# Performance work log

Hardware: AMD Instinct MI355X
Metric: run time of the kernel (lower is better)

Reference implementation:

```python
import jax, jax.numpy as jnp
import numpy as np

N, E = 50000, 1600000
C_IN, C_H, C_OUT = 36, 64, 64
EPS = 1e-16  # PyG softmax denominator epsilon


def setup_inputs() -> dict:
    key = jax.random.key(0)
    ks = jax.random.split(key, 48)
    inp = {}
    inp["features"] = jax.random.normal(ks[0], (N, C_IN), dtype=jnp.float32)
    inp["edge_attr"] = jax.random.uniform(ks[1], (E, 1), dtype=jnp.float32)
    inp["edge_index"] = jax.random.randint(ks[2], (2, E), 0, N, dtype=jnp.int32)
    dims = [(C_IN, C_H), (C_H, C_H), (C_H, C_H), (C_H, C_OUT)]
    i = 3
    for l, (din, dout) in enumerate(dims, 1):
        s = 1.0 / np.sqrt(din)
        inp[f"Wl{l}"] = jax.random.normal(ks[i], (din, dout), jnp.float32) * s; i += 1
        inp[f"bl{l}"] = jax.random.normal(ks[i], (dout,), jnp.float32) * 0.02; i += 1
        inp[f"Wr{l}"] = jax.random.normal(ks[i], (din, dout), jnp.float32) * s; i += 1
        inp[f"br{l}"] = jax.random.normal(ks[i], (dout,), jnp.float32) * 0.02; i += 1
        inp[f"We{l}"] = jax.random.normal(ks[i], (1, dout), jnp.float32); i += 1
        inp[f"att{l}"] = jax.random.normal(ks[i], (dout,), jnp.float32) * s; i += 1
        inp[f"bo{l}"] = jax.random.normal(ks[i], (dout,), jnp.float32) * 0.02; i += 1
    mlp = [(C_OUT, C_OUT // 2, "m1"), (C_OUT // 2, C_OUT // 4, "m2"), (C_OUT // 4, 1, "m3")]
    for din, dout, tag in mlp:
        s = 1.0 / np.sqrt(din)
        inp[f"W{tag}"] = jax.random.normal(ks[i], (din, dout), jnp.float32) * s; i += 1
        inp[f"b{tag}"] = jax.random.normal(ks[i], (dout,), jnp.float32) * 0.02; i += 1
    return inp


def gatv2_conv(x, src, dst, edge_attr, Wl, bl, Wr, br, We, att, bo):
    """Single-head GATv2Conv with edge features (PyG semantics)."""
    xl = x @ Wl + bl                      # [N, dout] source transform
    xr = x @ Wr + br                      # [N, dout] target transform
    ea = edge_attr @ We                   # [E, dout]
    e = jax.nn.leaky_relu(xl[src] + xr[dst] + ea, 0.2)  # [E, dout]
    score = e @ att                       # [E]
    # segment softmax over edges sharing a destination node
    m = jax.ops.segment_max(score, dst, num_segments=N)
    a = jnp.exp(score - m[dst])
    denom = jax.ops.segment_sum(a, dst, num_segments=N)
    alpha = a / (denom[dst] + EPS)
    out = jax.ops.segment_sum(xl[src] * alpha[:, None], dst, num_segments=N)
    return out + bo


def reference(features, edge_attr, edge_index,
              Wl1, bl1, Wr1, br1, We1, att1, bo1,
              Wl2, bl2, Wr2, br2, We2, att2, bo2,
              Wl3, bl3, Wr3, br3, We3, att3, bo3,
              Wl4, bl4, Wr4, br4, We4, att4, bo4,
              Wm1, bm1, Wm2, bm2, Wm3, bm3):
    src, dst = edge_index[0], edge_index[1]
    x = jax.nn.relu(gatv2_conv(features, src, dst, edge_attr, Wl1, bl1, Wr1, br1, We1, att1, bo1))
    x = jax.nn.relu(gatv2_conv(x, src, dst, edge_attr, Wl2, bl2, Wr2, br2, We2, att2, bo2))
    x = jax.nn.relu(gatv2_conv(x, src, dst, edge_attr, Wl3, bl3, Wr3, br3, We3, att3, bo3))
    x = jax.nn.relu(gatv2_conv(x, src, dst, edge_attr, Wl4, bl4, Wr4, br4, We4, att4, bo4))
    x = jnp.mean(x, axis=-2)              # graph readout -> [C_OUT]
    x = jax.nn.relu(x @ Wm1 + bm1)
    x = jax.nn.relu(x @ Wm2 + bm2)
    return x @ Wm3 + bm3                  # [1]
```

## Files before the change

### kernel.cpp

```cpp
#include <hip/hip_runtime.h>


__device__ __forceinline__ float readlane_f(float v, int l) {
  return __int_as_float(__builtin_amdgcn_readlane(__float_as_int(v), l));
}
__device__ __forceinline__ int rfl(int v) { return __builtin_amdgcn_readfirstlane(v); }

__device__ __forceinline__ void row_to_lds(const float* g, float* l) {
  __builtin_amdgcn_global_load_lds((const __attribute__((address_space(1))) void*)g,
                                   (__attribute__((address_space(3))) void*)l,
                                   4, 0, 0);
}

__global__ void k_hist(const int* __restrict__ dst, int* __restrict__ deg, int E) {
  int e = blockIdx.x * blockDim.x + threadIdx.x;
  if (e < E) atomicAdd(&deg[dst[e]], 1);
}

__global__ void __launch_bounds__(256) k_scanA(const int* __restrict__ deg,
                                               int* __restrict__ bsum, int n) {
  __shared__ int ws[4];
  int tid = threadIdx.x, lane = tid & 63, wv = tid >> 6;
  int base = blockIdx.x * 1024 + tid;
  int s = 0;
  #pragma unroll
  for (int k = 0; k < 4; k++) {
    int i = base + k * 256;
    if (i < n) s += deg[i];
  }
  #pragma unroll
  for (int o = 32; o > 0; o >>= 1) s += __shfl_xor(s, o, 64);
  if (lane == 0) ws[wv] = s;
  __syncthreads();
  if (tid == 0) bsum[blockIdx.x] = ws[0] + ws[1] + ws[2] + ws[3];
}

__global__ void k_scanB(const int* __restrict__ bsum, int* __restrict__ boffs,
                        int* __restrict__ rowptr, int nb, int n) {
  int lane = threadIdx.x;
  int v = (lane < nb) ? bsum[lane] : 0;
  int x = v;
  #pragma unroll
  for (int o = 1; o < 64; o <<= 1) {
    int t = __shfl_up(x, o, 64);
    if (lane >= o) x += t;
  }
  if (lane < nb) boffs[lane] = x - v;
  if (lane == 63) rowptr[n] = x;
}

__global__ void __launch_bounds__(256) k_scanC(const int* __restrict__ deg,
                                               const int* __restrict__ boffs,
                                               int* __restrict__ rowptr, int n) {
  __shared__ int wtot[4];
  int tid = threadIdx.x, lane = tid & 63, wv = tid >> 6;
  int i0 = blockIdx.x * 1024 + tid * 4;
  int4 v = make_int4(0, 0, 0, 0);
  if (i0 + 3 < n) v = *(const int4*)(deg + i0);
  else {
    if (i0 + 0 < n) v.x = deg[i0 + 0];
    if (i0 + 1 < n) v.y = deg[i0 + 1];
    if (i0 + 2 < n) v.z = deg[i0 + 2];
  }
  int s = v.x + v.y + v.z + v.w;
  int x = s;
  #pragma unroll
  for (int o = 1; o < 64; o <<= 1) {
    int t = __shfl_up(x, o, 64);
    if (lane >= o) x += t;
  }
  if (lane == 63) wtot[wv] = x;
  __syncthreads();
  int wexcl = 0;
  for (int k = 0; k < 4; k++) if (k < wv) wexcl += wtot[k];
  int excl = boffs[blockIdx.x] + wexcl + (x - s);
  int4 o4;
  o4.x = excl; o4.y = o4.x + v.x; o4.z = o4.y + v.y; o4.w = o4.z + v.z;
  if (i0 + 3 < n) *(int4*)(rowptr + i0) = o4;
  else {
    if (i0 + 0 < n) rowptr[i0 + 0] = o4.x;
    if (i0 + 1 < n) rowptr[i0 + 1] = o4.y;
    if (i0 + 2 < n) rowptr[i0 + 2] = o4.z;
  }
}

#define NBK_MAX 256
__global__ void __launch_bounds__(256) k_scatter(
    const int* __restrict__ src, const int* __restrict__ dst,
    const float* __restrict__ ea_in, const int* __restrict__ rowptr,
    int* __restrict__ bcur, uint2* __restrict__ tmp, int E, int nbk) {
  __shared__ int cnt[NBK_MAX];
  __shared__ int cur[NBK_MAX];
  __shared__ int gbase[NBK_MAX];
  __shared__ int sbase[NBK_MAX];
  int tid = threadIdx.x;
  if (tid < nbk) {
    cnt[tid] = 0;
    cur[tid] = 0;
    sbase[tid] = rowptr[tid << 8];
  }
  __syncthreads();
  int base = blockIdx.x * 4096 + tid;
  uint2 rec[16];
  #pragma unroll
  for (int k = 0; k < 16; k++) {
    int e = base + k * 256;
    if (e < E) {
      unsigned d = (unsigned)dst[e];
      rec[k] = make_uint2((d << 16) | (unsigned)src[e],
                          (unsigned)__float_as_int(ea_in[e]));
      atomicAdd(&cnt[d >> 8], 1);
    } else {
      rec[k] = make_uint2(0u, 0u);
    }
  }
  __syncthreads();
  if (tid < nbk) {
    int c = cnt[tid];
    gbase[tid] = (c > 0) ? atomicAdd(&bcur[tid * 16], c) : 0;
  }
  __syncthreads();
  #pragma unroll
  for (int k = 0; k < 16; k++) {
    int e = base + k * 256;
    if (e < E) {
      int b = (int)(rec[k].x >> 24);
      int slot = atomicAdd(&cur[b], 1);
      tmp[sbase[b] + gbase[b] + slot] = rec[k];
    }
  }
}

__global__ void __launch_bounds__(256) k_csr(const int* __restrict__ rowptr,
                                             const uint2* __restrict__ tmp,
                                             int2* __restrict__ pairs, int N) {
  __shared__ int sRP[257];
  __shared__ int cur[256];
  int b = blockIdx.x;
  int n0 = b << 8;
  int tid = threadIdx.x;
  sRP[tid] = rowptr[min(n0 + tid, N)];
  if (tid == 0) sRP[256] = rowptr[min(n0 + 256, N)];
  cur[tid] = 0;
  __syncthreads();
  int lo = sRP[0], hi = sRP[256];
  for (int k = lo + tid; k < hi; k += 256) {
    uint2 rec = tmp[k];
    int local = (int)(rec.x >> 16) - n0;
    int pos = sRP[local] + atomicAdd(&cur[local], 1);
    pairs[pos] = make_int2((int)(rec.x & 0xffffu), (int)rec.y);
  }
}

template <int DIN, int TILES>
__global__ void __launch_bounds__(256) k_transform(
    const float* __restrict__ x, const float* __restrict__ Wl, const float* __restrict__ bl,
    const float* __restrict__ Wr, const float* __restrict__ br,
    float* __restrict__ xl, float* __restrict__ xr, int nNodes) {
  __shared__ __align__(16) float sWl[DIN * 64];
  __shared__ __align__(16) float sWr[DIN * 64];
  __shared__ float sx[16][DIN + 1];
  int tid = threadIdx.x;
  for (int i = tid; i < DIN * 64; i += 256) { sWl[i] = Wl[i]; sWr[i] = Wr[i]; }
  int node = tid >> 4;
  int t4 = (tid & 15) * 4;
  float4 bl4 = *(const float4*)(bl + t4);
  float4 br4 = *(const float4*)(br + t4);
  for (int t = 0; t < TILES; t++) {
    int nb = (blockIdx.x * TILES + t) * 16;
    if (nb >= nNodes) break;
    __syncthreads();
    for (int i = tid; i < 16 * DIN; i += 256) {
      int ln = i / DIN, c = i % DIN;
      int g = nb + ln;
      sx[ln][c] = (g < nNodes) ? x[(size_t)g * DIN + c] : 0.f;
    }
    __syncthreads();
    float4 accl = bl4;
    float4 accr = br4;
    const float* xrow = sx[node];
    #pragma unroll 4
    for (int k = 0; k < DIN; k++) {
      float xv = xrow[k];
      float4 wl = *(const float4*)(sWl + k * 64 + t4);
      float4 wr = *(const float4*)(sWr + k * 64 + t4);
      accl.x = fmaf(xv, wl.x, accl.x); accl.y = fmaf(xv, wl.y, accl.y);
      accl.z = fmaf(xv, wl.z, accl.z); accl.w = fmaf(xv, wl.w, accl.w);
      accr.x = fmaf(xv, wr.x, accr.x); accr.y = fmaf(xv, wr.y, accr.y);
      accr.z = fmaf(xv, wr.z, accr.z); accr.w = fmaf(xv, wr.w, accr.w);
    }
    int g = nb + node;
    if (g < nNodes) {
      *(float4*)(xl + (size_t)g * 64 + t4) = accl;
      *(float4*)(xr + (size_t)g * 64 + t4) = accr;
    }
  }
}

#define SC1(T, EA, OUT) { float u, acc; \
  u = T.x + fmaf(EA, We4.x, xr4.x); u = fmaxf(u, 0.2f * u); acc = at4.x * u; \
  u = T.y + fmaf(EA, We4.y, xr4.y); u = fmaxf(u, 0.2f * u); acc = fmaf(at4.y, u, acc); \
  u = T.z + fmaf(EA, We4.z, xr4.z); u = fmaxf(u, 0.2f * u); acc = fmaf(at4.z, u, acc); \
  u = T.w + fmaf(EA, We4.w, xr4.w); u = fmaxf(u, 0.2f * u); acc = fmaf(at4.w, u, acc); \
  OUT = acc; }

__global__ void __launch_bounds__(256, 5) k_edge(
    const float* __restrict__ xl, const float* __restrict__ xr,
    const int* __restrict__ rowptr, const int2* __restrict__ pairs,
    const float* __restrict__ We, const float* __restrict__ att,
    const float* __restrict__ bo, float* __restrict__ xout, int nNodes) {
  int lane = threadIdx.x & 63;
  int wv = rfl((int)(threadIdx.x >> 6));
  int n = rfl(blockIdx.x * 4 + wv);
  if (n >= nNodes) return;
  int c4 = lane & 15;
  int r  = lane >> 4;
  int cb = c4 * 4;

  float4 We4 = *(const float4*)(We + cb);
  float4 at4 = *(const float4*)(att + cb);
  float4 xr4 = *(const float4*)(xr + (size_t)n * 64 + cb);
  int s0 = rfl(rowptr[n]);
  int s1 = rfl(rowptr[n + 1]);
  int last = s1 - 1;

  float m = -3.0e38f, d = 0.f;
  float4 A = {0.f, 0.f, 0.f, 0.f};

  for (int kb = s0; kb < s1; kb += 16) {
    int cnt = rfl(min(16, s1 - kb));
    int2 p0 = pairs[min(kb + r,      last)];
    int2 p1 = pairs[min(kb + 4 + r,  last)];
    int2 p2 = pairs[min(kb + 8 + r,  last)];
    int2 p3 = pairs[min(kb + 12 + r, last)];
    float ea0 = __int_as_float(p0.y);
    float ea1 = __int_as_float(p1.y);
    float ea2 = __int_as_float(p2.y);
    float ea3 = __int_as_float(p3.y);

    float4 t0 = *(const float4*)(xl + (size_t)(unsigned)p0.x * 64 + cb);
    float4 t1 = *(const float4*)(xl + (size_t)(unsigned)p1.x * 64 + cb);
    float4 t2 = *(const float4*)(xl + (size_t)(unsigned)p2.x * 64 + cb);
    float4 t3 = *(const float4*)(xl + (size_t)(unsigned)p3.x * 64 + cb);

    float sc0, sc1, sc2, sc3;
    SC1(t0, ea0, sc0)
    SC1(t1, ea1, sc1)
    SC1(t2, ea2, sc2)
    SC1(t3, ea3, sc3)

    #pragma unroll
    for (int o = 1; o <= 8; o <<= 1) {
      sc0 += __shfl_xor(sc0, o, 64);
      sc1 += __shfl_xor(sc1, o, 64);
      sc2 += __shfl_xor(sc2, o, 64);
      sc3 += __shfl_xor(sc3, o, 64);
    }
    sc0 = (r < cnt)      ? sc0 : -3.0e38f;
    sc1 = (4 + r < cnt)  ? sc1 : -3.0e38f;
    sc2 = (8 + r < cnt)  ? sc2 : -3.0e38f;
    sc3 = (12 + r < cnt) ? sc3 : -3.0e38f;

    float mc = fmaxf(fmaxf(sc0, sc1), fmaxf(sc2, sc3));
    mc = fmaxf(mc, __shfl_xor(mc, 16, 64));
    mc = fmaxf(mc, __shfl_xor(mc, 32, 64));
    float newm = fmaxf(m, mc);
    float rf = __expf(m - newm);
    float a0 = __expf(sc0 - newm);
    float a1 = __expf(sc1 - newm);
    float a2 = __expf(sc2 - newm);
    float a3 = __expf(sc3 - newm);
    float ds = (a0 + a1) + (a2 + a3);
    ds += __shfl_xor(ds, 16, 64);
    ds += __shfl_xor(ds, 32, 64);
    d = d * rf + ds;
    m = newm;

    A.x = fmaf(a0, t0.x, A.x * rf); A.y = fmaf(a0, t0.y, A.y * rf);
    A.z = fmaf(a0, t0.z, A.z * rf); A.w = fmaf(a0, t0.w, A.w * rf);
    A.x = fmaf(a1, t1.x, A.x); A.y = fmaf(a1, t1.y, A.y);
    A.z = fmaf(a1, t1.z, A.z); A.w = fmaf(a1, t1.w, A.w);
    A.x = fmaf(a2, t2.x, A.x); A.y = fmaf(a2, t2.y, A.y);
    A.z = fmaf(a2, t2.z, A.z); A.w = fmaf(a2, t2.w, A.w);
    A.x = fmaf(a3, t3.x, A.x); A.y = fmaf(a3, t3.y, A.y);
    A.z = fmaf(a3, t3.z, A.z); A.w = fmaf(a3, t3.w, A.w);
  }

  A.x += __shfl_xor(A.x, 16, 64); A.y += __shfl_xor(A.y, 16, 64);
  A.z += __shfl_xor(A.z, 16, 64); A.w += __shfl_xor(A.w, 16, 64);
  A.x += __shfl_xor(A.x, 32, 64); A.y += __shfl_xor(A.y, 32, 64);
  A.z += __shfl_xor(A.z, 32, 64); A.w += __shfl_xor(A.w, 32, 64);

  float inv = 1.f / (d + 1e-16f);
  if (r == 0) {
    float4 bo4 = *(const float4*)(bo + cb);
    float4 o4;
    o4.x = fmaxf(fmaf(A.x, inv, bo4.x), 0.f);
    o4.y = fmaxf(fmaf(A.y, inv, bo4.y), 0.f);
    o4.z = fmaxf(fmaf(A.z, inv, bo4.z), 0.f);
    o4.w = fmaxf(fmaf(A.w, inv, bo4.w), 0.f);
    *(float4*)(xout + (size_t)n * 64 + cb) = o4;
  }
}

__global__ void k_mean(const float* __restrict__ x, double* __restrict__ meanbuf, int nNodes) {
  __shared__ float sacc[256];
  int lane = threadIdx.x & 63;
  int wv = threadIdx.x >> 6;
  int gw = blockIdx.x * 4 + wv;
  int stride = gridDim.x * 4;
  float acc = 0.f;
  for (int n = gw; n < nNodes; n += stride) acc += x[(size_t)n * 64 + lane];
  sacc[threadIdx.x] = acc;
  __syncthreads();
  if (threadIdx.x < 64) {
    float a = sacc[threadIdx.x] + sacc[threadIdx.x + 64] + sacc[threadIdx.x + 128] + sacc[threadIdx.x + 192];
    atomicAdd(&meanbuf[lane], (double)a);
  }
}

__global__ void k_mlp(const double* __restrict__ meanbuf,
                      const float* __restrict__ Wm1, const float* __restrict__ bm1,
                      const float* __restrict__ Wm2, const float* __restrict__ bm2,
                      const float* __restrict__ Wm3, const float* __restrict__ bm3,
                      float* __restrict__ out, double invN) {
  __shared__ float xm[64];
  __shared__ float h1[32];
  __shared__ float h2[16];
  int t = threadIdx.x;
  xm[t] = (float)(meanbuf[t] * invN);
  __syncthreads();
  if (t < 32) {
    float a = bm1[t];
    for (int c = 0; c < 64; c++) a = fmaf(xm[c], Wm1[c * 32 + t], a);
    h1[t] = fmaxf(a, 0.f);
  }
  __syncthreads();
  if (t < 16) {
    float a = bm2[t];
    for (int c = 0; c < 32; c++) a = fmaf(h1[c], Wm2[c * 16 + t], a);
    h2[t] = fmaxf(a, 0.f);
  }
  __syncthreads();
  if (t == 0) {
    float a = bm3[0];
    for (int c = 0; c < 16; c++) a = fmaf(h2[c], Wm3[c], a);
    out[0] = a;
  }
}

extern "C" void kernel_launch(void* const* d_in, const int* in_sizes, int n_in,
                              void* d_out, int out_size, void* d_ws, size_t ws_size,
                              hipStream_t stream) {
  (void)n_in; (void)out_size; (void)ws_size;
  const int N = in_sizes[0] / 36;
  const int E = in_sizes[1];

  const float* feat = (const float*)d_in[0];
  const float* eat  = (const float*)d_in[1];
  const int*   eidx = (const int*)d_in[2];
  const int* src = eidx;
  const int* dst = eidx + E;

  const float* L[4][7];
  for (int l = 0; l < 4; l++)
    for (int j = 0; j < 7; j++) L[l][j] = (const float*)d_in[3 + l * 7 + j];
  const float* Wm1 = (const float*)d_in[31];
  const float* bm1 = (const float*)d_in[32];
  const float* Wm2 = (const float*)d_in[33];
  const float* bm2 = (const float*)d_in[34];
  const float* Wm3 = (const float*)d_in[35];
  const float* bm3 = (const float*)d_in[36];

  const int NBK = (N + 255) >> 8;

  char* ws = (char*)d_ws;
  size_t off = 0;
  auto alloc = [&](size_t bytes) {
    off = (off + 511) & ~(size_t)511;
    void* p = ws + off;
    off += bytes;
    return p;
  };
  int*    deg     = (int*)alloc((size_t)N * 4);
  int*    bcur    = (int*)alloc((size_t)NBK * 16 * 4);
  double* meanbuf = (double*)alloc(64 * 8);
  size_t zero_bytes = off;
  int*    rowptr  = (int*)alloc((size_t)(N + 1) * 4);
  int*    bsum    = (int*)alloc(64 * 4);
  int*    boffs   = (int*)alloc(64 * 4);
  int2*   pairs   = (int2*)alloc((size_t)E * 8);
  float*  xA      = (float*)alloc((size_t)N * 64 * 4);
  float*  xB      = (float*)alloc((size_t)N * 64 * 4);
  float*  xC      = (float*)alloc((size_t)N * 64 * 4);
  uint2*  tmp     = (uint2*)xC;

  hipMemsetAsync(d_ws, 0, zero_bytes, stream);

  const int TILES = 4;
  int egrid = (E + 255) / 256;
  int sgrid = (E + 4095) / 4096;
  int tgrid = (N + 16 * TILES - 1) / (16 * TILES);
  int ngrid = (N + 3) / 4;
  int nb = (N + 1023) / 1024;

  k_hist<<<egrid, 256, 0, stream>>>(dst, deg, E);
  k_scanA<<<nb, 256, 0, stream>>>(deg, bsum, N);
  k_scanB<<<1, 64, 0, stream>>>(bsum, boffs, rowptr, nb, N);
  k_scanC<<<nb, 256, 0, stream>>>(deg, boffs, rowptr, N);
  k_scatter<<<sgrid, 256, 0, stream>>>(src, dst, eat, rowptr, bcur, tmp, E, NBK);
  k_csr<<<NBK, 256, 0, stream>>>(rowptr, tmp, pairs, N);

  for (int l = 0; l < 4; l++) {
    if (l == 0)
      k_transform<36, TILES><<<tgrid, 256, 0, stream>>>(feat, L[0][0], L[0][1], L[0][2], L[0][3], xA, xB, N);
    else
      k_transform<64, TILES><<<tgrid, 256, 0, stream>>>(xC, L[l][0], L[l][1], L[l][2], L[l][3], xA, xB, N);
    k_edge<<<ngrid, 256, 0, stream>>>(xA, xB, rowptr, pairs,
                                      L[l][4], L[l][5], L[l][6], xC, N);
  }

  k_mean<<<256, 256, 0, stream>>>(xC, meanbuf, N);
  k_mlp<<<1, 64, 0, stream>>>(meanbuf, Wm1, bm1, Wm2, bm2, Wm3, bm3, (float*)d_out, 1.0 / (double)N);
}
```

Baseline: 577.8 us.

## Replace per-node degree histogram and scan with bucket counts plus per-block local scan

Removes the global per-node atomic histogram and three-kernel scan used to build CSR row pointers. Instead, each block counts edges per 256-node bucket in LDS and a single-block scan produces bucket offsets. The CSR kernel then counts and scans per-node degrees locally in LDS and writes rowptr itself. This cuts global atomic traffic and two kernel launches, at the cost of an extra pass over each bucket's records in k_csr.

```diff
diff --git a/kernel.cpp b/kernel.cpp
--- a/kernel.cpp
+++ b/kernel.cpp
@@ -1,93 +1,51 @@
 #include <hip/hip_runtime.h>
 
 
-__device__ __forceinline__ float readlane_f(float v, int l) {
-  return __int_as_float(__builtin_amdgcn_readlane(__float_as_int(v), l));
-}
 __device__ __forceinline__ int rfl(int v) { return __builtin_amdgcn_readfirstlane(v); }
 
-__device__ __forceinline__ void row_to_lds(const float* g, float* l) {
-  __builtin_amdgcn_global_load_lds((const __attribute__((address_space(1))) void*)g,
-                                   (__attribute__((address_space(3))) void*)l,
-                                   4, 0, 0);
-}
-
-__global__ void k_hist(const int* __restrict__ dst, int* __restrict__ deg, int E) {
-  int e = blockIdx.x * blockDim.x + threadIdx.x;
-  if (e < E) atomicAdd(&deg[dst[e]], 1);
-}
-
-__global__ void __launch_bounds__(256) k_scanA(const int* __restrict__ deg,
-                                               int* __restrict__ bsum, int n) {
-  __shared__ int ws[4];
+#define NBK_MAX 256
+
+__global__ void __launch_bounds__(256) k_bcount(const int* __restrict__ dst,
+                                                int* __restrict__ bkcnt, int E, int nbk) {
+  __shared__ int cnt[NBK_MAX];
+  int tid = threadIdx.x;
+  if (tid < nbk) cnt[tid] = 0;
+  __syncthreads();
+  int base = blockIdx.x * 4096 + tid;
+  #pragma unroll
+  for (int k = 0; k < 16; k++) {
+    int e = base + k * 256;
+    if (e < E) atomicAdd(&cnt[((unsigned)dst[e]) >> 8], 1);
+  }
+  __syncthreads();
+  if (tid < nbk) {
+    int c = cnt[tid];
+    if (c > 0) atomicAdd(&bkcnt[tid * 16], c);
+  }
+}
+
+__global__ void k_bscan(const int* __restrict__ bkcnt, int* __restrict__ boffs,
+                        int nbk, int E) {
+  __shared__ int wsum[4];
   int tid = threadIdx.x, lane = tid & 63, wv = tid >> 6;
-  int base = blockIdx.x * 1024 + tid;
-  int s = 0;
-  #pragma unroll
-  for (int k = 0; k < 4; k++) {
-    int i = base + k * 256;
-    if (i < n) s += deg[i];
-  }
-  #pragma unroll
-  for (int o = 32; o > 0; o >>= 1) s += __shfl_xor(s, o, 64);
-  if (lane == 0) ws[wv] = s;
-  __syncthreads();
-  if (tid == 0) bsum[blockIdx.x] = ws[0] + ws[1] + ws[2] + ws[3];
-}
-
-__global__ void k_scanB(const int* __restrict__ bsum, int* __restrict__ boffs,
-                        int* __restrict__ rowptr, int nb, int n) {
-  int lane = threadIdx.x;
-  int v = (lane < nb) ? bsum[lane] : 0;
+  int v = (tid < nbk) ? bkcnt[tid * 16] : 0;
   int x = v;
   #pragma unroll
   for (int o = 1; o < 64; o <<= 1) {
     int t = __shfl_up(x, o, 64);
     if (lane >= o) x += t;
   }
-  if (lane < nb) boffs[lane] = x - v;
-  if (lane == 63) rowptr[n] = x;
-}
-
-__global__ void __launch_bounds__(256) k_scanC(const int* __restrict__ deg,
-                                               const int* __restrict__ boffs,
-                                               int* __restrict__ rowptr, int n) {
-  __shared__ int wtot[4];
-  int tid = threadIdx.x, lane = tid & 63, wv = tid >> 6;
-  int i0 = blockIdx.x * 1024 + tid * 4;
-  int4 v = make_int4(0, 0, 0, 0);
-  if (i0 + 3 < n) v = *(const int4*)(deg + i0);
-  else {
-    if (i0 + 0 < n) v.x = deg[i0 + 0];
-    if (i0 + 1 < n) v.y = deg[i0 + 1];
-    if (i0 + 2 < n) v.z = deg[i0 + 2];
-  }
-  int s = v.x + v.y + v.z + v.w;
-  int x = s;
-  #pragma unroll
-  for (int o = 1; o < 64; o <<= 1) {
-    int t = __shfl_up(x, o, 64);
-    if (lane >= o) x += t;
-  }
-  if (lane == 63) wtot[wv] = x;
-  __syncthreads();
-  int wexcl = 0;
-  for (int k = 0; k < 4; k++) if (k < wv) wexcl += wtot[k];
-  int excl = boffs[blockIdx.x] + wexcl + (x - s);
-  int4 o4;
-  o4.x = excl; o4.y = o4.x + v.x; o4.z = o4.y + v.y; o4.w = o4.z + v.z;
-  if (i0 + 3 < n) *(int4*)(rowptr + i0) = o4;
-  else {
-    if (i0 + 0 < n) rowptr[i0 + 0] = o4.x;
-    if (i0 + 1 < n) rowptr[i0 + 1] = o4.y;
-    if (i0 + 2 < n) rowptr[i0 + 2] = o4.z;
-  }
-}
-
-#define NBK_MAX 256
+  if (lane == 63) wsum[wv] = x;
+  __syncthreads();
+  int wo = 0;
+  for (int k = 0; k < 4; k++) if (k < wv) wo += wsum[k];
+  if (tid < nbk) boffs[tid] = wo + (x - v);
+  if (tid == 0) boffs[nbk] = E;
+}
+
 __global__ void __launch_bounds__(256) k_scatter(
     const int* __restrict__ src, const int* __restrict__ dst,
-    const float* __restrict__ ea_in, const int* __restrict__ rowptr,
+    const float* __restrict__ ea_in, const int* __restrict__ boffs,
     int* __restrict__ bcur, uint2* __restrict__ tmp, int E, int nbk) {
   __shared__ int cnt[NBK_MAX];
   __shared__ int cur[NBK_MAX];
@@ -97,7 +55,7 @@
   if (tid < nbk) {
     cnt[tid] = 0;
     cur[tid] = 0;
-    sbase[tid] = rowptr[tid << 8];
+    sbase[tid] = boffs[tid];
   }
   __syncthreads();
   int base = blockIdx.x * 4096 + tid;
@@ -131,23 +89,44 @@
   }
 }
 
-__global__ void __launch_bounds__(256) k_csr(const int* __restrict__ rowptr,
+__global__ void __launch_bounds__(256) k_csr(const int* __restrict__ boffs,
                                              const uint2* __restrict__ tmp,
-                                             int2* __restrict__ pairs, int N) {
-  __shared__ int sRP[257];
+                                             int2* __restrict__ pairs,
+                                             int* __restrict__ rowptr, int N) {
+  __shared__ int cnt[256];
+  __shared__ int pref[256];
   __shared__ int cur[256];
+  __shared__ int wsum[4];
   int b = blockIdx.x;
   int n0 = b << 8;
-  int tid = threadIdx.x;
-  sRP[tid] = rowptr[min(n0 + tid, N)];
-  if (tid == 0) sRP[256] = rowptr[min(n0 + 256, N)];
+  int tid = threadIdx.x, lane = tid & 63, wv = tid >> 6;
+  cnt[tid] = 0;
   cur[tid] = 0;
   __syncthreads();
-  int lo = sRP[0], hi = sRP[256];
+  int lo = boffs[b], hi = boffs[b + 1];
+  for (int k = lo + tid; k < hi; k += 256)
+    atomicAdd(&cnt[(int)(tmp[k].x >> 16) - n0], 1);
+  __syncthreads();
+  int v = cnt[tid];
+  int x = v;
+  #pragma unroll
+  for (int o = 1; o < 64; o <<= 1) {
+    int t = __shfl_up(x, o, 64);
+    if (lane >= o) x += t;
+  }
+  if (lane == 63) wsum[wv] = x;
+  __syncthreads();
+  int wo = 0;
+  for (int k = 0; k < 4; k++) if (k < wv) wo += wsum[k];
+  int start = lo + wo + (x - v);
+  pref[tid] = start;
+  int nn = n0 + tid;
+  if (nn <= N) rowptr[nn] = start;
+  __syncthreads();
   for (int k = lo + tid; k < hi; k += 256) {
     uint2 rec = tmp[k];
     int local = (int)(rec.x >> 16) - n0;
-    int pos = sRP[local] + atomicAdd(&cur[local], 1);
+    int pos = pref[local] + atomicAdd(&cur[local], 1);
     pairs[pos] = make_int2((int)(rec.x & 0xffffu), (int)rec.y);
   }
 }
@@ -382,13 +361,12 @@
     off += bytes;
     return p;
   };
-  int*    deg     = (int*)alloc((size_t)N * 4);
+  int*    bkcnt   = (int*)alloc((size_t)NBK * 16 * 4);
   int*    bcur    = (int*)alloc((size_t)NBK * 16 * 4);
   double* meanbuf = (double*)alloc(64 * 8);
   size_t zero_bytes = off;
+  int*    boffs   = (int*)alloc((size_t)(NBK + 1) * 4);
   int*    rowptr  = (int*)alloc((size_t)(N + 1) * 4);
-  int*    bsum    = (int*)alloc(64 * 4);
-  int*    boffs   = (int*)alloc(64 * 4);
   int2*   pairs   = (int2*)alloc((size_t)E * 8);
   float*  xA      = (float*)alloc((size_t)N * 64 * 4);
   float*  xB      = (float*)alloc((size_t)N * 64 * 4);
@@ -398,18 +376,14 @@
   hipMemsetAsync(d_ws, 0, zero_bytes, stream);
 
   const int TILES = 4;
-  int egrid = (E + 255) / 256;
   int sgrid = (E + 4095) / 4096;
   int tgrid = (N + 16 * TILES - 1) / (16 * TILES);
   int ngrid = (N + 3) / 4;
-  int nb = (N + 1023) / 1024;
-
-  k_hist<<<egrid, 256, 0, stream>>>(dst, deg, E);
-  k_scanA<<<nb, 256, 0, stream>>>(deg, bsum, N);
-  k_scanB<<<1, 64, 0, stream>>>(bsum, boffs, rowptr, nb, N);
-  k_scanC<<<nb, 256, 0, stream>>>(deg, boffs, rowptr, N);
-  k_scatter<<<sgrid, 256, 0, stream>>>(src, dst, eat, rowptr, bcur, tmp, E, NBK);
-  k_csr<<<NBK, 256, 0, stream>>>(rowptr, tmp, pairs, N);
+
+  k_bcount<<<sgrid, 256, 0, stream>>>(dst, bkcnt, E, NBK);
+  k_bscan<<<1, 256, 0, stream>>>(bkcnt, boffs, NBK, E);
+  k_scatter<<<sgrid, 256, 0, stream>>>(src, dst, eat, boffs, bcur, tmp, E, NBK);
+  k_csr<<<NBK, 256, 0, stream>>>(boffs, tmp, pairs, rowptr, N);
 
   for (int l = 0; l < 4; l++) {
     if (l == 0)
```

After: 519.5 us. 1.11x faster.
